# Kernel optimization log

Hardware: AMD Instinct MI355X
Metric: run time of the kernel (lower is better)

## Reference

```python
import jax, jax.numpy as jnp
import numpy as np

B, T, D_MODEL, WINDOW = 2, 2048, 512, 32


def setup_inputs() -> dict:
    key = jax.random.key(0)
    ks = jax.random.split(key, 5)
    s = 1.0 / np.sqrt(D_MODEL)
    x = jax.random.normal(ks[0], (B, T, D_MODEL), jnp.float32)
    # torch.nn.Linear convention: weight [out_features, in_features], y = x @ W.T + b
    w_qkv = jax.random.uniform(ks[1], (3 * D_MODEL, D_MODEL), jnp.float32, -s, s)
    b_qkv = jax.random.uniform(ks[2], (3 * D_MODEL,), jnp.float32, -s, s)
    w_proj = jax.random.uniform(ks[3], (D_MODEL, D_MODEL), jnp.float32, -s, s)
    b_proj = jax.random.uniform(ks[4], (D_MODEL,), jnp.float32, -s, s)
    return {"x": x, "w_qkv": w_qkv, "b_qkv": b_qkv, "w_proj": w_proj, "b_proj": b_proj}


def reference(x, w_qkv, b_qkv, w_proj, b_proj):
    Bb, Tt, C = x.shape
    qkv = x @ w_qkv.T + b_qkv                      # [B,T,3C]
    q, k, v = jnp.split(qkv, 3, axis=-1)           # each [B,T,C]
    W = 2 * WINDOW - 1                             # non-causal window span [t-w+1, t+w-1]
    offs = jnp.arange(W) - (WINDOW - 1)            # [W]
    idx = jnp.arange(Tt)[:, None] + offs[None, :]  # [T,W] absolute key positions
    valid = (idx >= 0) & (idx < Tt)                # mask out-of-range window slots
    idx_c = jnp.clip(idx, 0, Tt - 1)
    k_win = k[:, idx_c]                            # [B,T,W,C]
    v_win = v[:, idx_c]                            # [B,T,W,C]
    scale = jnp.asarray(C, x.dtype) ** 0.5
    scores = jnp.einsum('btc,btwc->btw', q, k_win) / scale
    scores = jnp.where(valid[None], scores, -jnp.inf)
    p = jax.nn.softmax(scores, axis=-1)            # [B,T,W]
    out = jnp.einsum('btw,btwc->btc', p, v_win)    # [B,T,C]
    return out @ w_proj.T + b_proj
```

## Files before the change

kernel.cpp:

```cpp
#include <hip/hip_runtime.h>
#include <math.h>

#define BB 2
#define TT 2048
#define CC 512
#define WIN 32
#define WSZ 63
#define MM (BB * TT)

typedef __attribute__((ext_vector_type(8))) short short8;
typedef __attribute__((ext_vector_type(4))) float floatx4;

__device__ inline unsigned short bf16_rn(float f) {
  unsigned u = __builtin_bit_cast(unsigned, f);
  u += 0x7fff + ((u >> 16) & 1);
  return (unsigned short)(u >> 16);
}
__device__ inline unsigned pack_bf16x2(float lo, float hi) {
  return (unsigned)bf16_rn(lo) | ((unsigned)bf16_rn(hi) << 16);
}

#define NX  (MM * CC)
#define NWQ (3 * CC * CC)
#define NWP (CC * CC)

__global__ __launch_bounds__(256) void convert_bf16(
    const float* __restrict__ x, const float* __restrict__ wq,
    const float* __restrict__ wp, ushort* __restrict__ xb,
    ushort* __restrict__ wqb, ushort* __restrict__ wpb) {
  const size_t e = ((size_t)blockIdx.x * 256 + threadIdx.x) * 8;
  const float* src;
  ushort* dst;
  size_t off;
  if (e < NX) { src = x; dst = xb; off = e; }
  else if (e < NX + NWQ) { src = wq; dst = wqb; off = e - NX; }
  else { src = wp; dst = wpb; off = e - NX - NWQ; }
  float4 v0 = ((const float4*)(src + off))[0];
  float4 v1 = ((const float4*)(src + off))[1];
  uint4 o;
  o.x = pack_bf16x2(v0.x, v0.y);
  o.y = pack_bf16x2(v0.z, v0.w);
  o.z = pack_bf16x2(v1.x, v1.y);
  o.w = pack_bf16x2(v1.z, v1.w);
  *(uint4*)(dst + off) = o;
}

#define PSTR 264
#define VSTR 136

template <int BM, typename OT>
__global__ __launch_bounds__(256) void gemm_panel(
    const ushort* __restrict__ A, const ushort* __restrict__ B,
    const float* __restrict__ bias, OT* __restrict__ C,
    ushort* __restrict__ VT, int M, int N) {
  constexpr int MIW = BM / 64;
  __shared__ __align__(16) ushort Bs[64 * PSTR];

  const int tid = threadIdx.x;
  const int lane = tid & 63;
  const int wave = tid >> 6;
  const int m0 = blockIdx.y * BM;
  const int n0 = blockIdx.x * 64;
  const int wm = wave * (BM / 4);
  const int mlane = lane & 15, quad = lane >> 4;

  floatx4 acc[MIW][4];
#pragma unroll
  for (int i = 0; i < MIW; ++i)
#pragma unroll
    for (int j = 0; j < 4; ++j) acc[i][j] = (floatx4){0.f, 0.f, 0.f, 0.f};

  for (int h = 0; h < 2; ++h) {
    if (h) __syncthreads();
#pragma unroll
    for (int i = 0; i < 8; ++i) {
      const int idx = tid + 256 * i;
      const int r = idx >> 5, kc = (idx & 31) * 8;
      *(uint4*)(&Bs[r * PSTR + kc]) =
          *(const uint4*)(B + (size_t)(n0 + r) * CC + h * 256 + kc);
    }
    __syncthreads();
#pragma unroll
    for (int ks = 0; ks < 8; ++ks) {
      short8 bfr[4];
#pragma unroll
      for (int ni = 0; ni < 4; ++ni)
        bfr[ni] = *(const short8*)(&Bs[(ni * 16 + mlane) * PSTR + ks * 32 + quad * 8]);
#pragma unroll
      for (int mi = 0; mi < MIW; ++mi) {
        short8 af = *(const short8*)(
            A + (size_t)(m0 + wm + mi * 16 + mlane) * CC + h * 256 + ks * 32 + quad * 8);
#pragma unroll
        for (int ni = 0; ni < 4; ++ni)
          acc[mi][ni] = __builtin_amdgcn_mfma_f32_16x16x32_bf16(af, bfr[ni], acc[mi][ni], 0, 0, 0);
      }
    }
  }

  const bool vpath = (VT != nullptr) && (n0 >= 1024);
  if (!vpath) {
#pragma unroll
    for (int ni = 0; ni < 4; ++ni) {
      const int n = n0 + ni * 16 + mlane;
      const float bn = bias[n];
#pragma unroll
      for (int mi = 0; mi < MIW; ++mi) {
        const int mbase = m0 + wm + mi * 16 + quad * 4;
#pragma unroll
        for (int r = 0; r < 4; ++r) {
          float val = acc[mi][ni][r] + bn;
          if constexpr (sizeof(OT) == 2)
            ((ushort*)C)[(size_t)(mbase + r) * N + n] = bf16_rn(val);
          else
            ((float*)C)[(size_t)(mbase + r) * N + n] = val;
        }
      }
    }
  } else if constexpr (BM == 128) {
    ushort* Vt = Bs;
    __syncthreads();
#pragma unroll
    for (int ni = 0; ni < 4; ++ni) {
      const int n_l = ni * 16 + mlane;
      const float bn = bias[n0 + n_l];
#pragma unroll
      for (int mi = 0; mi < MIW; ++mi) {
        const int m_l = wm + mi * 16 + quad * 4;
        ushort4 pk;
        pk.x = bf16_rn(acc[mi][ni][0] + bn);
        pk.y = bf16_rn(acc[mi][ni][1] + bn);
        pk.z = bf16_rn(acc[mi][ni][2] + bn);
        pk.w = bf16_rn(acc[mi][ni][3] + bn);
        *(ushort4*)(&Vt[n_l * VSTR + m_l]) = pk;
      }
    }
    __syncthreads();
#pragma unroll
    for (int i = 0; i < 4; ++i) {
      const int idx = tid + 256 * i;
      const int n_l = idx >> 4, mo = (idx & 15) * 8;
      *(uint4*)(VT + (size_t)(n0 - 1024 + n_l) * M + m0 + mo) =
          *(const uint4*)(&Vt[n_l * VSTR + mo]);
    }
  }
}

#define ATILE 16
#define SLD 84
#define PLD 104

__global__ __launch_bounds__(256) void attn_mfma(
    const ushort* __restrict__ qkv, const ushort* __restrict__ vT,
    ushort* __restrict__ out) {
  __shared__ __align__(16) float s_s[16 * SLD];
  __shared__ __align__(16) ushort p_s[16 * PLD];

  const int tid = threadIdx.x;
  const int wave = tid >> 6, lane = tid & 63;
  const int mlane = lane & 15, quad = lane >> 4;
  const int tile = ((blockIdx.x & 7) << 5) | (blockIdx.x >> 3);
  const int bt0 = tile * ATILE;
  const int b = bt0 / TT, t0 = bt0 % TT;
  const ushort* qbase = qkv + (size_t)b * TT * (3 * CC);

  const ushort* qrow  = qbase + (ptrdiff_t)(t0 + mlane) * (3 * CC);
  const ushort* krow0 = qbase + (ptrdiff_t)(t0 - 32 + wave * 16 + mlane) * (3 * CC) + CC;
  const ushort* krow1 = qbase + (ptrdiff_t)(t0 - 32 + 64 + mlane) * (3 * CC) + CC;
  floatx4 sacc0 = (floatx4){0.f, 0.f, 0.f, 0.f};
  floatx4 sacc1 = (floatx4){0.f, 0.f, 0.f, 0.f};
#pragma unroll
  for (int ks = 0; ks < 16; ++ks) {
    short8 a  = *(const short8*)(qrow + ks * 32 + quad * 8);
    short8 b0 = *(const short8*)(krow0 + ks * 32 + quad * 8);
    sacc0 = __builtin_amdgcn_mfma_f32_16x16x32_bf16(a, b0, sacc0, 0, 0, 0);
    if (wave == 0) {
      short8 b1 = *(const short8*)(krow1 + ks * 32 + quad * 8);
      sacc1 = __builtin_amdgcn_mfma_f32_16x16x32_bf16(a, b1, sacc1, 0, 0, 0);
    }
  }

#pragma unroll
  for (int r = 0; r < 4; ++r)
    s_s[(quad * 4 + r) * SLD + wave * 16 + mlane] = sacc0[r];
  if (wave == 0) {
#pragma unroll
    for (int r = 0; r < 4; ++r)
      s_s[(quad * 4 + r) * SLD + 64 + mlane] = sacc1[r];
  }
  __syncthreads();

  {
    const int row = tid >> 4, li = tid & 15;
    const float inv_scale = 0.044194173824159216f;
    float e[5];
    float mx = -INFINITY;
#pragma unroll
    for (int i = 0; i < 5; ++i) {
      const int r = li + 16 * i;
      const int j = r - 1 - row;
      const int src = t0 - 32 + r;
      const bool valid = (j >= 0) && (j < WSZ) && (src >= 0) && (src < TT);
      e[i] = valid ? s_s[row * SLD + r] * inv_scale : -INFINITY;
      mx = fmaxf(mx, e[i]);
    }
    mx = fmaxf(mx, __shfl_xor(mx, 1)); mx = fmaxf(mx, __shfl_xor(mx, 2));
    mx = fmaxf(mx, __shfl_xor(mx, 4)); mx = fmaxf(mx, __shfl_xor(mx, 8));
    float sum = 0.f;
#pragma unroll
    for (int i = 0; i < 5; ++i) {
      e[i] = (e[i] == -INFINITY) ? 0.f : __expf(e[i] - mx);
      sum += e[i];
    }
    sum += __shfl_xor(sum, 1); sum += __shfl_xor(sum, 2);
    sum += __shfl_xor(sum, 4); sum += __shfl_xor(sum, 8);
    const float rs = 1.f / sum;
#pragma unroll
    for (int i = 0; i < 5; ++i)
      p_s[row * PLD + li + 16 * i] = bf16_rn(e[i] * rs);
    if (li < 8) {
      p_s[row * PLD + 80 + li] = 0;
      p_s[row * PLD + 88 + li] = 0;
      p_s[row * PLD + 96 + li] = 0;
    }
  }
  __syncthreads();

  const ptrdiff_t mcol0 = (ptrdiff_t)b * TT + t0 - 32;
#pragma unroll 2
  for (int nt8 = 0; nt8 < 8; ++nt8) {
    const int nt = wave * 8 + nt8;
    const ushort* vrow = vT + (ptrdiff_t)(nt * 16 + mlane) * MM + mcol0;
    floatx4 o = (floatx4){0.f, 0.f, 0.f, 0.f};
#pragma unroll
    for (int ks = 0; ks < 3; ++ks) {
      short8 a  = *(const short8*)(&p_s[mlane * PLD + ks * 32 + quad * 8]);
      short8 bv = *(const short8*)(vrow + ks * 32 + quad * 8);
      o = __builtin_amdgcn_mfma_f32_16x16x32_bf16(a, bv, o, 0, 0, 0);
    }
#pragma unroll
    for (int r = 0; r < 4; ++r)
      out[(size_t)(bt0 + quad * 4 + r) * CC + nt * 16 + mlane] = bf16_rn(o[r]);
  }
}

extern "C" void kernel_launch(void* const* d_in, const int* in_sizes, int n_in,
                              void* d_out, int out_size, void* d_ws, size_t ws_size,
                              hipStream_t stream) {
  const float* x      = (const float*)d_in[0];
  const float* w_qkv  = (const float*)d_in[1];
  const float* b_qkv  = (const float*)d_in[2];
  const float* w_proj = (const float*)d_in[3];
  const float* b_proj = (const float*)d_in[4];
  float* outp = (float*)d_out;

  ushort* base  = (ushort*)d_ws;
  ushort* qkv   = base + 131072;
  ushort* attn  = qkv + (size_t)MM * 3 * CC;
  ushort* xb    = attn + (size_t)MM * CC;
  ushort* wqb   = xb + (size_t)NX;
  ushort* wpb   = wqb + (size_t)NWQ;
  ushort* vTg   = wpb + (size_t)NWP;
  ushort* vT    = vTg + 64;

  convert_bf16<<<(NX + NWQ + NWP) / (256 * 8), 256, 0, stream>>>(x, w_qkv, w_proj, xb, wqb, wpb);
  {
    dim3 grid((3 * CC) / 64, MM / 128);
    gemm_panel<128, ushort><<<grid, 256, 0, stream>>>(xb, wqb, b_qkv, qkv, vT, MM, 3 * CC);
  }
  attn_mfma<<<MM / ATILE, 256, 0, stream>>>(qkv, vT, attn);
  {
    dim3 grid(CC / 64, MM / 64);
    gemm_panel<64, float><<<grid, 256, 0, stream>>>(attn, wpb, b_proj, outp, nullptr, MM, CC);
  }
}
```

Measured before the change: 109.2 us.

## Fuse output projection GEMM into windowed attention kernel

The attention output tile (16 rows x 512) is now staged as bf16 in shared memory, and the same block multiplies it by the projection weights, adding the bias and writing fp32 output directly. This removes the separate projection GEMM launch and the round trip of the attention output through global memory. In exchange each 16-row block streams the full 512x512 projection weight from global/L2, so weight reads grow, and extra registers (16 short8 A fragments) plus more LDS per block may reduce occupancy.

```diff
diff --git a/kernel.cpp b/kernel.cpp
--- a/kernel.cpp
+++ b/kernel.cpp
@@ -48,20 +48,19 @@
 #define PSTR 264
 #define VSTR 136
 
-template <int BM, typename OT>
-__global__ __launch_bounds__(256) void gemm_panel(
+__global__ __launch_bounds__(256) void gemm_qkv(
     const ushort* __restrict__ A, const ushort* __restrict__ B,
-    const float* __restrict__ bias, OT* __restrict__ C,
+    const float* __restrict__ bias, ushort* __restrict__ C,
     ushort* __restrict__ VT, int M, int N) {
-  constexpr int MIW = BM / 64;
+  constexpr int MIW = 2;
   __shared__ __align__(16) ushort Bs[64 * PSTR];
 
   const int tid = threadIdx.x;
   const int lane = tid & 63;
   const int wave = tid >> 6;
-  const int m0 = blockIdx.y * BM;
+  const int m0 = blockIdx.y * 128;
   const int n0 = blockIdx.x * 64;
-  const int wm = wave * (BM / 4);
+  const int wm = wave * 32;
   const int mlane = lane & 15, quad = lane >> 4;
 
   floatx4 acc[MIW][4];
@@ -97,7 +96,7 @@
     }
   }
 
-  const bool vpath = (VT != nullptr) && (n0 >= 1024);
+  const bool vpath = (n0 >= 1024);
   if (!vpath) {
 #pragma unroll
     for (int ni = 0; ni < 4; ++ni) {
@@ -107,16 +106,11 @@
       for (int mi = 0; mi < MIW; ++mi) {
         const int mbase = m0 + wm + mi * 16 + quad * 4;
 #pragma unroll
-        for (int r = 0; r < 4; ++r) {
-          float val = acc[mi][ni][r] + bn;
-          if constexpr (sizeof(OT) == 2)
-            ((ushort*)C)[(size_t)(mbase + r) * N + n] = bf16_rn(val);
-          else
-            ((float*)C)[(size_t)(mbase + r) * N + n] = val;
-        }
+        for (int r = 0; r < 4; ++r)
+          C[(size_t)(mbase + r) * N + n] = bf16_rn(acc[mi][ni][r] + bn);
       }
     }
-  } else if constexpr (BM == 128) {
+  } else {
     ushort* Vt = Bs;
     __syncthreads();
 #pragma unroll
@@ -148,12 +142,15 @@
 #define ATILE 16
 #define SLD 84
 #define PLD 104
-
-__global__ __launch_bounds__(256) void attn_mfma(
+#define OLD 520
+
+__global__ __launch_bounds__(256) void attn_proj(
     const ushort* __restrict__ qkv, const ushort* __restrict__ vT,
-    ushort* __restrict__ out) {
+    const ushort* __restrict__ wp, const float* __restrict__ bproj,
+    float* __restrict__ outp) {
   __shared__ __align__(16) float s_s[16 * SLD];
   __shared__ __align__(16) ushort p_s[16 * PLD];
+  __shared__ __align__(16) ushort o_s[16 * OLD];
 
   const int tid = threadIdx.x;
   const int wave = tid >> 6, lane = tid & 63;
@@ -239,7 +236,28 @@
     }
 #pragma unroll
     for (int r = 0; r < 4; ++r)
-      out[(size_t)(bt0 + quad * 4 + r) * CC + nt * 16 + mlane] = bf16_rn(o[r]);
+      o_s[(quad * 4 + r) * OLD + nt * 16 + mlane] = bf16_rn(o[r]);
+  }
+  __syncthreads();
+
+  short8 afr[16];
+#pragma unroll
+  for (int ks = 0; ks < 16; ++ks)
+    afr[ks] = *(const short8*)(&o_s[mlane * OLD + ks * 32 + quad * 8]);
+#pragma unroll
+  for (int nt2 = 0; nt2 < 8; ++nt2) {
+    const int n = wave * 128 + nt2 * 16 + mlane;
+    const ushort* wrow = wp + (size_t)n * CC;
+    floatx4 acc = (floatx4){0.f, 0.f, 0.f, 0.f};
+#pragma unroll
+    for (int ks = 0; ks < 16; ++ks) {
+      short8 bfr = *(const short8*)(wrow + ks * 32 + quad * 8);
+      acc = __builtin_amdgcn_mfma_f32_16x16x32_bf16(afr[ks], bfr, acc, 0, 0, 0);
+    }
+    const float bn = bproj[n];
+#pragma unroll
+    for (int r = 0; r < 4; ++r)
+      outp[(size_t)(bt0 + quad * 4 + r) * CC + n] = acc[r] + bn;
   }
 }
 
@@ -255,21 +273,18 @@
 
   ushort* base  = (ushort*)d_ws;
   ushort* qkv   = base + 131072;
-  ushort* attn  = qkv + (size_t)MM * 3 * CC;
-  ushort* xb    = attn + (size_t)MM * CC;
+  ushort* guard = qkv + (size_t)MM * 3 * CC;
+  ushort* xb    = guard + (size_t)MM * CC;
   ushort* wqb   = xb + (size_t)NX;
   ushort* wpb   = wqb + (size_t)NWQ;
   ushort* vTg   = wpb + (size_t)NWP;
   ushort* vT    = vTg + 64;
+  (void)guard;
 
   convert_bf16<<<(NX + NWQ + NWP) / (256 * 8), 256, 0, stream>>>(x, w_qkv, w_proj, xb, wqb, wpb);
   {
     dim3 grid((3 * CC) / 64, MM / 128);
-    gemm_panel<128, ushort><<<grid, 256, 0, stream>>>(xb, wqb, b_qkv, qkv, vT, MM, 3 * CC);
-  }
-  attn_mfma<<<MM / ATILE, 256, 0, stream>>>(qkv, vT, attn);
-  {
-    dim3 grid(CC / 64, MM / 64);
-    gemm_panel<64, float><<<grid, 256, 0, stream>>>(attn, wpb, b_proj, outp, nullptr, MM, CC);
-  }
-}
+    gemm_qkv<<<grid, 256, 0, stream>>>(xb, wqb, b_qkv, qkv, vT, MM, 3 * CC);
+  }
+  attn_proj<<<MM / ATILE, 256, 0, stream>>>(qkv, vT, wpb, b_proj, outp);
+}
```

After: 117.9 us. 8.0% more time.
